# Kernel tuning notes

Hardware: AMD Instinct MI355X
Metric: run time of the kernel (lower is better)

Reference implementation:

```python
import jax, jax.numpy as jnp
import numpy as np

N_QUBITS = 4
N_LAYERS = 3
N_OUTPUTS = 4
BATCH = 1048576


def _ry(t):
    # RY(t) = [[cos(t/2), -sin(t/2)], [sin(t/2), cos(t/2)]]; t may be scalar or (B,)
    c = jnp.cos(t / 2)
    s = jnp.sin(t / 2)
    m = jnp.stack([jnp.stack([c, -s], -1), jnp.stack([s, c], -1)], -2)
    return m.astype(jnp.complex64)


def _rx(t):
    c = jnp.cos(t / 2).astype(jnp.complex64)
    s = jnp.sin(t / 2).astype(jnp.complex64)
    return jnp.stack([jnp.stack([c, -1j * s], -1), jnp.stack([-1j * s, c], -1)], -2)


def _rz(t):
    e = jnp.exp(-1j * t.astype(jnp.complex64) / 2)  # exp(-i t/2)
    z = jnp.zeros_like(e)
    return jnp.stack([jnp.stack([e, z], -1), jnp.stack([z, jnp.conj(e)], -1)], -2)


def _apply_1q(state, U, q):
    # shared 2x2 gate U on wire q; state: (B, 2,2,2,2)
    s = jnp.moveaxis(state, q + 1, -1)
    s = jnp.einsum('ij,...j->...i', U, s)
    return jnp.moveaxis(s, -1, q + 1)


def _apply_1q_batched(state, U, q):
    # per-sample 2x2 gate U: (B,2,2) on wire q
    s = jnp.moveaxis(state, q + 1, -1)  # (B, ..., 2)
    s = jnp.einsum('bij,b...j->b...i', U, s)
    return jnp.moveaxis(s, -1, q + 1)


def _apply_cnot(state, c, t):
    s = jnp.moveaxis(state, (c + 1, t + 1), (-2, -1))  # (..., ctrl, tgt)
    s = jnp.stack([s[..., 0, :], s[..., 1, ::-1]], axis=-2)
    return jnp.moveaxis(s, (-2, -1), (c + 1, t + 1))


def setup_inputs() -> dict:
    key = jax.random.key(0)
    kx, kw = jax.random.split(key)
    x = jax.random.normal(kx, (BATCH, 2), dtype=jnp.float32)
    weights = jax.random.normal(kw, (N_LAYERS, N_QUBITS, 3), dtype=jnp.float32) * 0.1
    return {"x": x, "weights": weights}


def reference(x, weights):
    B = x.shape[0]
    # |0...0> state, batched
    state = jnp.zeros((B,) + (2,) * N_QUBITS, jnp.complex64)
    state = state.at[(slice(None),) + (0,) * N_QUBITS].set(1.0)
    # data encoding: RY(inputs[i % 2]) on wire i (per-sample angles)
    for i in range(N_QUBITS):
        state = _apply_1q_batched(state, _ry(x[:, i % 2]), i)
    # variational layers (shared angles)
    for l in range(N_LAYERS):
        for i in range(N_QUBITS):
            state = _apply_1q(state, _rx(weights[l, i, 0]), i)
            state = _apply_1q(state, _ry(weights[l, i, 1]), i)
            state = _apply_1q(state, _rz(weights[l, i, 2]), i)
        for i in range(N_QUBITS):
            state = _apply_cnot(state, i, (i + 1) % N_QUBITS)
    probs = state.real ** 2 + state.imag ** 2  # (B,2,2,2,2)
    outs = []
    for q in range(N_OUTPUTS):
        p = jnp.moveaxis(probs, q + 1, 1).reshape(B, 2, -1).sum(-1)
        outs.append(p[:, 0] - p[:, 1])  # <Z_q>
    return jnp.stack(outs, -1)  # (B, N_OUTPUTS)
```

## Files before the change

kernel.cpp:

```cpp
#include <hip/hip_runtime.h>
#include <hip/hip_bf16.h>


__device__ __forceinline__ float2 mul2(float2 a, float2 b) {
    return make_float2(a.x * b.x, a.y * b.y);
}
__device__ __forceinline__ float2 fma2(float s, float2 a, float2 b) {
    return make_float2(fmaf(s, a.x, b.x), fmaf(s, a.y, b.y));
}

__global__ __launch_bounds__(256) void qnn_fused(const float2* __restrict__ x2,
                                                 const float* __restrict__ w,
                                                 float4* __restrict__ out,
                                                 int B) {
    __shared__ float Ur[16][16];
    __shared__ float Ui[16][16];
    __shared__ float gs[36];
    __shared__ float gc[36];
    __shared__ __align__(16) float Csh[100];
    const int t = threadIdx.x;

    if (t < 100) Csh[t] = 0.0f;
    if (t < 36) {
        const float th = w[t] * 0.5f;
        gs[t] = __sinf(th);
        gc[t] = __cosf(th);
    }
    __syncthreads();

    if (t < 16) {
        float ar[16], ai[16];
#pragma unroll
        for (int i = 0; i < 16; i++) { ar[i] = (i == t) ? 1.0f : 0.0f; ai[i] = 0.0f; }

#pragma unroll
        for (int l = 0; l < 3; l++) {
#pragma unroll
            for (int wq = 0; wq < 4; wq++) {
                const int st = 1 << (3 - wq);
                const int g0 = (l * 4 + wq) * 3;
                const float sx = gs[g0 + 0], cx = gc[g0 + 0];
                const float sy = gs[g0 + 1], cy = gc[g0 + 1];
                const float sz = gs[g0 + 2], cz = gc[g0 + 2];
#pragma unroll
                for (int lo = 0; lo < 16; lo++) if (!(lo & st)) {
                    const int hi = lo | st;
                    const float arl = ar[lo], ail = ai[lo], arh = ar[hi], aih = ai[hi];
                    ar[lo] = cx * arl + sx * aih;
                    ai[lo] = cx * ail - sx * arh;
                    ar[hi] = cx * arh + sx * ail;
                    ai[hi] = cx * aih - sx * arl;
                }
#pragma unroll
                for (int lo = 0; lo < 16; lo++) if (!(lo & st)) {
                    const int hi = lo | st;
                    const float arl = ar[lo], ail = ai[lo], arh = ar[hi], aih = ai[hi];
                    ar[lo] = cy * arl - sy * arh;
                    ai[lo] = cy * ail - sy * aih;
                    ar[hi] = sy * arl + cy * arh;
                    ai[hi] = sy * ail + cy * aih;
                }
#pragma unroll
                for (int lo = 0; lo < 16; lo++) if (!(lo & st)) {
                    const int hi = lo | st;
                    const float arl = ar[lo], ail = ai[lo], arh = ar[hi], aih = ai[hi];
                    ar[lo] = cz * arl + sz * ail;
                    ai[lo] = cz * ail - sz * arl;
                    ar[hi] = cz * arh - sz * aih;
                    ai[hi] = cz * aih + sz * arh;
                }
            }
#pragma unroll
            for (int ci = 0; ci < 4; ci++) {
                const int cst = 1 << (3 - ci);
                const int tst = 1 << (3 - ((ci + 1) & 3));
#pragma unroll
                for (int k = 0; k < 16; k++) if ((k & cst) && !(k & tst)) {
                    const int k2 = k | tst;
                    const float tr = ar[k], ti = ai[k];
                    ar[k] = ar[k2]; ai[k] = ai[k2];
                    ar[k2] = tr;    ai[k2] = ti;
                }
            }
        }
#pragma unroll
        for (int i = 0; i < 16; i++) { Ur[i][t] = ar[i]; Ui[i][t] = ai[i]; }
    }
    __syncthreads();

    {
        const int i = t >> 4;
        const int j = t & 15;
        float m0 = 0.f, m1 = 0.f, m2 = 0.f, m3 = 0.f;
#pragma unroll
        for (int k = 0; k < 16; k++) {
            const float r = Ur[k][i] * Ur[k][j] + Ui[k][i] * Ui[k][j];
            m0 += ((k >> 3) & 1) ? -r : r;
            m1 += ((k >> 2) & 1) ? -r : r;
            m2 += ((k >> 1) & 1) ? -r : r;
            m3 += ((k >> 0) & 1) ? -r : r;
        }
        const int mm = ((i >> 3) & 1) + ((i >> 1) & 1) + ((j >> 3) & 1) + ((j >> 1) & 1);
        const int nn = ((i >> 2) & 1) + (i & 1) + ((j >> 2) & 1) + (j & 1);
        const int mn4 = (mm * 5 + nn) * 4;
        atomicAdd(&Csh[mn4 + 0], m0);
        atomicAdd(&Csh[mn4 + 1], m1);
        atomicAdd(&Csh[mn4 + 2], m2);
        atomicAdd(&Csh[mn4 + 3], m3);
    }
    __syncthreads();

    const float4* __restrict__ Csh4 = (const float4*)Csh;
    float4 cv[25];
#pragma unroll
    for (int i = 0; i < 25; i++) cv[i] = Csh4[i];

    const int bs = blockIdx.x * 1024;

    if (bs + 1024 <= B) {
        const int sA0 = bs + t;
        const float2 xA0 = x2[sA0];
        const float2 xB0 = x2[sA0 + 256];
        const float2 xA1 = x2[sA0 + 512];
        const float2 xB1 = x2[sA0 + 768];

#pragma unroll
        for (int k = 0; k < 2; k++) {
            const float2 xA = k ? xA1 : xA0;
            const float2 xB = k ? xB1 : xB0;
            const float2 s0 = make_float2(__sinf(xA.x * 0.5f), __sinf(xB.x * 0.5f));
            const float2 c0 = make_float2(__cosf(xA.x * 0.5f), __cosf(xB.x * 0.5f));
            const float2 s1 = make_float2(__sinf(xA.y * 0.5f), __sinf(xB.y * 0.5f));
            const float2 c1 = make_float2(__cosf(xA.y * 0.5f), __cosf(xB.y * 0.5f));

            const float2 cc0 = mul2(c0, c0), ss0 = mul2(s0, s0), cs0 = mul2(c0, s0);
            const float2 cc1 = mul2(c1, c1), ss1 = mul2(s1, s1), cs1 = mul2(c1, s1);
            const float2 p0[5] = { mul2(cc0, cc0), mul2(cc0, cs0), mul2(cs0, cs0),
                                   mul2(cs0, ss0), mul2(ss0, ss0) };
            const float2 p1[5] = { mul2(cc1, cc1), mul2(cc1, cs1), mul2(cs1, cs1),
                                   mul2(cs1, ss1), mul2(ss1, ss1) };

            float2 a0 = make_float2(0.f, 0.f), a1 = a0, a2 = a0, a3 = a0;
#pragma unroll
            for (int m = 0; m < 5; m++)
#pragma unroll
                for (int n = 0; n < 5; n++) {
                    const float4 cvv = cv[m * 5 + n];
                    const float2 pp = mul2(p0[m], p1[n]);
                    a0 = fma2(cvv.x, pp, a0);
                    a1 = fma2(cvv.y, pp, a1);
                    a2 = fma2(cvv.z, pp, a2);
                    a3 = fma2(cvv.w, pp, a3);
                }
            const int sA = bs + k * 512 + t;
            out[sA]       = make_float4(a0.x, a1.x, a2.x, a3.x);
            out[sA + 256] = make_float4(a0.y, a1.y, a2.y, a3.y);
        }
    } else {
#pragma unroll
        for (int k = 0; k < 4; k++) {
            const int s = bs + k * 256 + t;
            if (s < B) {
                const float2 xv = x2[s];
                const float st0 = __sinf(xv.x * 0.5f), ct0 = __cosf(xv.x * 0.5f);
                const float st1 = __sinf(xv.y * 0.5f), ct1 = __cosf(xv.y * 0.5f);
                const float cc0 = ct0 * ct0, ss0 = st0 * st0, cs0 = ct0 * st0;
                const float cc1 = ct1 * ct1, ss1 = st1 * st1, cs1 = ct1 * st1;
                const float q0[5] = { cc0 * cc0, cc0 * cs0, cs0 * cs0, cs0 * ss0, ss0 * ss0 };
                const float q1[5] = { cc1 * cc1, cc1 * cs1, cs1 * cs1, cs1 * ss1, ss1 * ss1 };
                float o0 = 0.f, o1 = 0.f, o2 = 0.f, o3 = 0.f;
#pragma unroll
                for (int m = 0; m < 5; m++)
#pragma unroll
                    for (int n = 0; n < 5; n++) {
                        const float4 cvv = cv[m * 5 + n];
                        const float pp = q0[m] * q1[n];
                        o0 = fmaf(cvv.x, pp, o0);
                        o1 = fmaf(cvv.y, pp, o1);
                        o2 = fmaf(cvv.z, pp, o2);
                        o3 = fmaf(cvv.w, pp, o3);
                    }
                out[s] = make_float4(o0, o1, o2, o3);
            }
        }
    }
}

extern "C" void kernel_launch(void* const* d_in, const int* in_sizes, int n_in,
                              void* d_out, int out_size, void* d_ws, size_t ws_size,
                              hipStream_t stream) {
    const float* x = (const float*)d_in[0];
    const float* w = (const float*)d_in[1];
    const int B = in_sizes[0] / 2;

    int grid = (B + 1023) / 1024;
    if (grid < 1) grid = 1;
    qnn_fused<<<grid, 256, 0, stream>>>((const float2*)x, w, (float4*)d_out, B);
}
```

Measured before the change: 79.20 us.

## Build circuit unitary with 256 threads using lane shuffles instead of 16 serial threads

The 16x16 circuit unitary is now computed with one matrix element per thread across all 256 threads. Gate pair exchanges use __shfl_xor within groups of 16 lanes, replacing the per-thread 16-element register arrays updated serially by only 16 threads. This shortens the per-block setup prologue, which runs before any sample is processed, at the cost of many cross-lane shuffle operations.

```diff
diff --git a/kernel.cpp b/kernel.cpp
--- a/kernel.cpp
+++ b/kernel.cpp
@@ -28,10 +28,11 @@
     }
     __syncthreads();
 
-    if (t < 16) {
-        float ar[16], ai[16];
-#pragma unroll
-        for (int i = 0; i < 16; i++) { ar[i] = (i == t) ? 1.0f : 0.0f; ai[i] = 0.0f; }
+    {
+        const int row = t & 15;
+        const int col = t >> 4;
+        float ar = (row == col) ? 1.0f : 0.0f;
+        float ai = 0.0f;
 
 #pragma unroll
         for (int l = 0; l < 3; l++) {
@@ -42,49 +43,40 @@
                 const float sx = gs[g0 + 0], cx = gc[g0 + 0];
                 const float sy = gs[g0 + 1], cy = gc[g0 + 1];
                 const float sz = gs[g0 + 2], cz = gc[g0 + 2];
-#pragma unroll
-                for (int lo = 0; lo < 16; lo++) if (!(lo & st)) {
-                    const int hi = lo | st;
-                    const float arl = ar[lo], ail = ai[lo], arh = ar[hi], aih = ai[hi];
-                    ar[lo] = cx * arl + sx * aih;
-                    ai[lo] = cx * ail - sx * arh;
-                    ar[hi] = cx * arh + sx * ail;
-                    ai[hi] = cx * aih - sx * arl;
+                {
+                    const float arp = __shfl_xor(ar, st);
+                    const float aip = __shfl_xor(ai, st);
+                    const float nar = cx * ar + sx * aip;
+                    const float nai = cx * ai - sx * arp;
+                    ar = nar; ai = nai;
                 }
-#pragma unroll
-                for (int lo = 0; lo < 16; lo++) if (!(lo & st)) {
-                    const int hi = lo | st;
-                    const float arl = ar[lo], ail = ai[lo], arh = ar[hi], aih = ai[hi];
-                    ar[lo] = cy * arl - sy * arh;
-                    ai[lo] = cy * ail - sy * aih;
-                    ar[hi] = sy * arl + cy * arh;
-                    ai[hi] = sy * ail + cy * aih;
+                {
+                    const float arp = __shfl_xor(ar, st);
+                    const float aip = __shfl_xor(ai, st);
+                    const float sgn = (row & st) ? sy : -sy;
+                    ar = cy * ar + sgn * arp;
+                    ai = cy * ai + sgn * aip;
                 }
-#pragma unroll
-                for (int lo = 0; lo < 16; lo++) if (!(lo & st)) {
-                    const int hi = lo | st;
-                    const float arl = ar[lo], ail = ai[lo], arh = ar[hi], aih = ai[hi];
-                    ar[lo] = cz * arl + sz * ail;
-                    ai[lo] = cz * ail - sz * arl;
-                    ar[hi] = cz * arh - sz * aih;
-                    ai[hi] = cz * aih + sz * arh;
+                {
+                    const float szl = (row & st) ? -sz : sz;
+                    const float nar = cz * ar + szl * ai;
+                    const float nai = cz * ai - szl * ar;
+                    ar = nar; ai = nai;
                 }
             }
 #pragma unroll
             for (int ci = 0; ci < 4; ci++) {
                 const int cst = 1 << (3 - ci);
                 const int tst = 1 << (3 - ((ci + 1) & 3));
-#pragma unroll
-                for (int k = 0; k < 16; k++) if ((k & cst) && !(k & tst)) {
-                    const int k2 = k | tst;
-                    const float tr = ar[k], ti = ai[k];
-                    ar[k] = ar[k2]; ai[k] = ai[k2];
-                    ar[k2] = tr;    ai[k2] = ti;
-                }
+                const float arp = __shfl_xor(ar, tst);
+                const float aip = __shfl_xor(ai, tst);
+                const bool sw = (row & cst) != 0;
+                ar = sw ? arp : ar;
+                ai = sw ? aip : ai;
             }
         }
-#pragma unroll
-        for (int i = 0; i < 16; i++) { Ur[i][t] = ar[i]; Ui[i][t] = ai[i]; }
+        Ur[row][col] = ar;
+        Ui[row][col] = ai;
     }
     __syncthreads();
 
```

Result: faster. 75.14 us (-5.1%).
